# Kernel optimization log

Hardware: AMD Instinct MI355X
Metric: run time of the kernel (lower is better)

## Reference

```python
import jax, jax.numpy as jnp
import numpy as np

# BEV projection config (from model_cfg.PROJECT_CFG)
PCR = np.array([0.0, -40.0, -3.0, 70.4, 40.0, 1.0], dtype=np.float32)
VOX = np.array([0.16, 0.16, 4.0], dtype=np.float32)
NX = int(round((PCR[3] - PCR[0]) / VOX[0]))  # 440
NY = int(round((PCR[4] - PCR[1]) / VOX[1]))  # 500
NVOX = NX * NY


def setup_inputs() -> dict:
    key = jax.random.key(0)
    ks = jax.random.split(key, 7)
    B, C, H, W = 2, 32, 32, 256
    fv = jax.random.normal(ks[0], (B, C, H, W), jnp.float32)
    lo = jnp.array([0.0, -40.0, -3.0], jnp.float32).reshape(1, 3, 1, 1)
    hi = jnp.array([70.4, 40.0, 1.0], jnp.float32).reshape(1, 3, 1, 1)

    def mk_pts(k1, k2):
        xyz = lo + jax.random.uniform(k1, (B, 3, H, W), jnp.float32) * (hi - lo)
        inten = jax.random.uniform(k2, (B, 1, H, W), jnp.float32)
        return jnp.concatenate([xyz, inten], axis=1)

    points_img = mk_pts(ks[1], ks[2])
    points_img_far = mk_pts(ks[3], ks[4])
    proj_masks = jax.random.randint(ks[5], (B, H, W), 0, 2).astype(jnp.int32)
    proj_masks_far = jax.random.randint(ks[6], (B, H, W), 0, 2).astype(jnp.int32)
    return {
        "fv_features": fv,
        "points_img": points_img,
        "points_img_far": points_img_far,
        "proj_masks": proj_masks,
        "proj_masks_far": proj_masks_far,
    }


def _bev_scatter(points, feats, valid):
    """Scatter-mean per-point features into the BEV grid.

    points: (M, 3), feats: (M, C), valid: (M,) bool. Invalid / out-of-range
    points go to an overflow bucket that is dropped.
    """
    ix = jnp.floor((points[:, 0] - PCR[0]) / VOX[0]).astype(jnp.int32)
    iy = jnp.floor((points[:, 1] - PCR[1]) / VOX[1]).astype(jnp.int32)
    inb = (ix >= 0) & (ix < NX) & (iy >= 0) & (iy < NY)
    inb = inb & (points[:, 2] >= PCR[2]) & (points[:, 2] < PCR[5])
    ok = valid & inb
    seg = jnp.where(ok, iy * NX + ix, NVOX)
    fsum = jax.ops.segment_sum(jnp.where(ok[:, None], feats, 0.0), seg,
                               num_segments=NVOX + 1)
    cnt = jax.ops.segment_sum(ok.astype(feats.dtype), seg,
                              num_segments=NVOX + 1)
    mean = fsum[:NVOX] / jnp.maximum(cnt[:NVOX], 1.0)[:, None]
    return mean.reshape(NY, NX, -1).transpose(2, 0, 1)  # (C, NY, NX)


def reference(fv_features, points_img, points_img_far, proj_masks, proj_masks_far):
    B, C, H, W = fv_features.shape
    N = H * W
    feats = fv_features.transpose(0, 2, 3, 1).reshape(B, N, C)
    pts = points_img[:, :3].transpose(0, 2, 3, 1).reshape(B, N, 3)
    ptsf = points_img_far[:, :3].transpose(0, 2, 3, 1).reshape(B, N, 3)
    m = proj_masks.reshape(B, N) > 0      # valid near points (knowns)
    mf = proj_masks_far.reshape(B, N) > 0  # valid far points (unknowns)

    # three_nn: squared distances from far points to valid near points
    d2 = jnp.sum((ptsf[:, :, None, :] - pts[:, None, :, :]) ** 2, axis=-1)  # (B,N,N)
    d2 = jnp.where(m[:, None, :], d2, jnp.inf)
    neg, idx = jax.lax.top_k(-d2, 3)  # (B,N,3) three nearest
    dist = -neg
    dist_recip = 1.0 / (dist + 1e-8)
    weight = dist_recip / jnp.sum(dist_recip, axis=-1, keepdims=True)  # (B,N,3)

    # three_interpolate: weighted gather of near features
    gathered = jnp.take_along_axis(
        feats, idx.reshape(B, N * 3)[:, :, None], axis=1).reshape(B, N, 3, C)
    interp = jnp.sum(gathered * weight[..., None], axis=2)  # (B,N,C)

    # cat([features, interpolated]), cat([points, points_far]) -> BEV scatter
    all_pts = jnp.concatenate([pts, ptsf], axis=1)       # (B, 2N, 3)
    all_feats = jnp.concatenate([feats, interp], axis=1)  # (B, 2N, C)
    all_valid = jnp.concatenate([m, mf], axis=1)          # (B, 2N)
    bev = jax.vmap(_bev_scatter)(all_pts, all_feats, all_valid)  # (B,C,NY,NX)
    return bev
```

## Files before the change

### kernel.cpp

```cpp
#include <hip/hip_runtime.h>

#define BB   2
#define CC   32
#define NN   8192
#define N2   (2 * NN)
#define NXv  440
#define NYv  500
#define NVOXv (NXv * NYv)

#define SPLIT 32
#define FPB   8

#define INSERT3(dd, jj)                                            \
    if ((dd) < d2) {                                               \
        if ((dd) < d1) {                                           \
            d2 = d1; i2 = i1;                                      \
            if ((dd) < d0) { d1 = d0; i1 = i0; d0 = (dd); i0 = (jj); } \
            else           { d1 = (dd); i1 = (jj); }               \
        } else { d2 = (dd); i2 = (jj); }                           \
    }

__global__ __launch_bounds__(256) void k_tr(
    const float* __restrict__ fv, float* __restrict__ F,
    int* __restrict__ counters)
{
    __shared__ float tile[CC][64 + 1];
    int b  = blockIdx.y;
    int i0 = blockIdx.x * 64;
    int t  = threadIdx.x;
    if (b == 0 && blockIdx.x == 0 && t < 4) counters[t] = 0;

    const float* f = fv + (size_t)b * CC * NN;
    int il = t & 63, cb = t >> 6;
#pragma unroll
    for (int p = 0; p < 8; ++p) {
        int c = cb + p * 4;
        tile[c][il] = f[(size_t)c * NN + i0 + il];
    }
    __syncthreads();
    float* o = F + ((size_t)b * N2 + i0) * CC;
    int c2 = t & 31, ib = t >> 5;
#pragma unroll
    for (int p = 0; p < 8; ++p) {
        int il2 = ib + p * 8;
        o[(size_t)il2 * CC + c2] = tile[c2][il2];
    }
}

__global__ __launch_bounds__(256) void k_prep(
    const float* __restrict__ pim,
    const float* __restrict__ pimf,
    const int*   __restrict__ pm,
    const int*   __restrict__ pmf,
    int*         __restrict__ head,
    int*         __restrict__ nxt,
    float4*      __restrict__ cand,
    int*         __restrict__ ccnt,
    float4*      __restrict__ fcand,
    int*         __restrict__ fcnt)
{
    int b = blockIdx.y;
    int i = blockIdx.x * blockDim.x + threadIdx.x;

    {
        float x = pimf[(b * 4 + 0) * NN + i];
        float y = pimf[(b * 4 + 1) * NN + i];
        float z = pimf[(b * 4 + 2) * NN + i];
        if (pmf[b * NN + i] > 0) {
            int ix = (int)floorf((x - 0.0f)  / 0.16f);
            int iy = (int)floorf((y + 40.0f) / 0.16f);
            if (ix >= 0 && ix < NXv && iy >= 0 && iy < NYv &&
                z >= -3.0f && z < 1.0f) {
                int vox = iy * NXv + ix;
                int pos = atomicAdd(&fcnt[b], 1);
                fcand[b * NN + pos] = make_float4(x, y, z, __int_as_float(vox));
            }
        }
    }

    if (pm[b * NN + i] > 0) {
        float x = pim[(b * 4 + 0) * NN + i];
        float y = pim[(b * 4 + 1) * NN + i];
        float z = pim[(b * 4 + 2) * NN + i];
        int pos = atomicAdd(&ccnt[b], 1);
        cand[b * NN + pos] = make_float4(x, y, z, __int_as_float(i));

        int ix = (int)floorf((x - 0.0f)  / 0.16f);
        int iy = (int)floorf((y + 40.0f) / 0.16f);
        if (ix < 0 || ix >= NXv || iy < 0 || iy >= NYv) return;
        if (!(z >= -3.0f && z < 1.0f)) return;
        int vox = iy * NXv + ix;
        nxt[b * N2 + i] = atomicExch(&head[b * NVOXv + vox], i);
    }
}

__global__ __launch_bounds__(256) void k_far(
    const float4* __restrict__ cand,
    const int*    __restrict__ ccnt,
    const float4* __restrict__ fcand,
    const int*    __restrict__ fcnt,
    float*        __restrict__ F,
    int*          __restrict__ head,
    int*          __restrict__ nxt)
{
    int b  = blockIdx.y;
    int nf = fcnt[b];
    int e0 = blockIdx.x * FPB;
    if (e0 >= nf) return;

    int tid = threadIdx.x;
    int sub = tid & (SPLIT - 1);
    int e   = e0 + (tid >> 5);
    if (e >= nf) return;

    float4 fp = fcand[b * NN + e];
    float x = fp.x, y = fp.y, z = fp.z;
    int vox = __float_as_int(fp.w);

    int nc = ccnt[b];
    const float4* cb = cand + b * NN;

    float d0 = __builtin_inff(), d1 = __builtin_inff(), d2 = __builtin_inff();
    int   i0 = 0, i1 = 0, i2 = 0;

    int k = sub;
    for (; k + 96 < nc; k += 128) {
        float4 pa = cb[k];
        float4 pb = cb[k + 32];
        float4 pc = cb[k + 64];
        float4 pd = cb[k + 96];
        float dxa = x - pa.x, dya = y - pa.y, dza = z - pa.z;
        float dxb = x - pb.x, dyb = y - pb.y, dzb = z - pb.z;
        float dxc = x - pc.x, dyc = y - pc.y, dzc = z - pc.z;
        float dxd = x - pd.x, dyd = y - pd.y, dzd = z - pd.z;
        float da = dxa * dxa + dya * dya + dza * dza;
        float db = dxb * dxb + dyb * dyb + dzb * dzb;
        float dc = dxc * dxc + dyc * dyc + dzc * dzc;
        float dd = dxd * dxd + dyd * dyd + dzd * dzd;
        int ia = __float_as_int(pa.w);
        int ib = __float_as_int(pb.w);
        int ic = __float_as_int(pc.w);
        int id = __float_as_int(pd.w);
        INSERT3(da, ia);
        INSERT3(db, ib);
        INSERT3(dc, ic);
        INSERT3(dd, id);
    }
    for (; k < nc; k += SPLIT) {
        float4 p = cb[k];
        float dx = x - p.x, dy = y - p.y, dz = z - p.z;
        float d  = dx * dx + dy * dy + dz * dz;
        int  ii  = __float_as_int(p.w);
        INSERT3(d, ii);
    }

#pragma unroll
    for (int off = 1; off < SPLIT; off <<= 1) {
        float m0 = __shfl_xor(d0, off), m1 = __shfl_xor(d1, off), m2 = __shfl_xor(d2, off);
        int   g0 = __shfl_xor(i0, off), g1 = __shfl_xor(i1, off), g2 = __shfl_xor(i2, off);
        INSERT3(m0, g0);
        INSERT3(m1, g1);
        INSERT3(m2, g2);
    }

    float r0 = 1.0f / (d0 + 1e-8f);
    float r1 = 1.0f / (d1 + 1e-8f);
    float r2 = 1.0f / (d2 + 1e-8f);
    float s  = r0 + r1 + r2;
    float w0 = r0 / s, w1 = r1 / s, w2 = r2 / s;

    const float* fb = F + ((size_t)b * N2 << 5);
    float v = w0 * fb[((size_t)i0 << 5) + sub] +
              w1 * fb[((size_t)i1 << 5) + sub] +
              w2 * fb[((size_t)i2 << 5) + sub];
    F[(((size_t)b * N2 + NN + e) << 5) + sub] = v;

    if (sub == 0)
        nxt[b * N2 + NN + e] = atomicExch(&head[b * NVOXv + vox], NN + e);
}

__global__ __launch_bounds__(256) void k_final(
    const float* __restrict__ F,
    const int*   __restrict__ head,
    const int*   __restrict__ nxt,
    float*       __restrict__ out)
{
    __shared__ float tile[CC][64 + 1];
    int b  = blockIdx.y;
    int v0 = blockIdx.x * 64;
    int t  = threadIdx.x;

    int vl = t >> 2, cq = (t & 3) * 8;
    int v  = v0 + vl;
    float acc[8] = {0, 0, 0, 0, 0, 0, 0, 0};
    if (v < NVOXv) {
        int p = head[b * NVOXv + v];
        int n = 0;
        while (p >= 0) {
            const float* f = F + (((size_t)b * N2 + p) << 5) + cq;
            float4 a0 = *(const float4*)f;
            float4 a1 = *(const float4*)(f + 4);
            acc[0] += a0.x; acc[1] += a0.y; acc[2] += a0.z; acc[3] += a0.w;
            acc[4] += a1.x; acc[5] += a1.y; acc[6] += a1.z; acc[7] += a1.w;
            ++n;
            p = nxt[b * N2 + p];
        }
        if (n > 1) {
            float cf = (float)n;
#pragma unroll
            for (int u = 0; u < 8; ++u) acc[u] /= cf;
        }
    }
#pragma unroll
    for (int u = 0; u < 8; ++u) tile[cq + u][vl] = acc[u];
    __syncthreads();

    int c = t >> 3, vb = (t & 7) * 8;
    if (v0 + vb < NVOXv) {
        float* o = out + (size_t)b * CC * NVOXv + (size_t)c * NVOXv + v0 + vb;
        *(float4*)(o)     = make_float4(tile[c][vb + 0], tile[c][vb + 1],
                                        tile[c][vb + 2], tile[c][vb + 3]);
        *(float4*)(o + 4) = make_float4(tile[c][vb + 4], tile[c][vb + 5],
                                        tile[c][vb + 6], tile[c][vb + 7]);
    }
}

extern "C" void kernel_launch(void* const* d_in, const int* in_sizes, int n_in,
                              void* d_out, int out_size, void* d_ws, size_t ws_size,
                              hipStream_t stream)
{
    const float* fv   = (const float*)d_in[0];
    const float* pim  = (const float*)d_in[1];
    const float* pimf = (const float*)d_in[2];
    const int*   pm   = (const int*)d_in[3];
    const int*   pmf  = (const int*)d_in[4];
    float* out = (float*)d_out;

    const size_t headB = (size_t)BB * NVOXv * sizeof(int);
    const size_t nxtB  = (size_t)BB * N2 * sizeof(int);
    const size_t candB = (size_t)BB * NN * sizeof(float4);
    const size_t FB    = (size_t)BB * N2 * CC * sizeof(float);

    char* ws = (char*)d_ws;
    int* counters = (int*)ws;
    size_t off = 256;
    int*    head  = (int*)(ws + off);   off += headB;
    int*    nxt   = (int*)(ws + off);   off += nxtB;
    float4* cand  = (float4*)(ws + off); off += candB;
    float4* fcand = (float4*)(ws + off); off += candB;
    float*  F     = (float*)(ws + off);  off += FB;
    (void)ws_size;

    hipMemsetAsync(head, 0xFF, headB, stream);

    dim3 blk(256);
    dim3 gt(NN / 64, BB);
    k_tr<<<gt, blk, 0, stream>>>(fv, F, counters);

    dim3 g1(NN / 256, BB);
    k_prep<<<g1, blk, 0, stream>>>(pim, pimf, pm, pmf, head, nxt,
                                   cand, counters, fcand, counters + 2);

    dim3 g2(NN / FPB, BB);
    k_far<<<g2, blk, 0, stream>>>(cand, counters, fcand, counters + 2,
                                  F, head, nxt);

    dim3 g3((NVOXv + 63) / 64, BB);
    k_final<<<g3, blk, 0, stream>>>(F, head, nxt, out);
}
```

Baseline: 126.1 us.

## Fuse transpose and prep kernels, halve k_far split width, fold counter init into memset

Merges the feature transpose kernel and the point preparation kernel into one launch. Only the first 64 threads of each block do the prep work, so one kernel launch is removed. Counters are now reset by the same 0xFF memset that clears the head array, with a -1+1 offset trick on the atomic counters. k_far now uses 16 lanes per far point instead of 32 and handles 16 points per block, so each lane scans twice as many candidates and writes two channels. This trades cross-lane reduction steps for more serial distance work per lane.

```diff
diff --git a/kernel.cpp b/kernel.cpp
--- a/kernel.cpp
+++ b/kernel.cpp
@@ -8,8 +8,8 @@
 #define NYv  500
 #define NVOXv (NXv * NYv)
 
-#define SPLIT 32
-#define FPB   8
+#define SPLIT 16
+#define FPB   16
 
 #define INSERT3(dd, jj)                                            \
     if ((dd) < d2) {                                               \
@@ -20,15 +20,23 @@
         } else { d2 = (dd); i2 = (jj); }                           \
     }
 
-__global__ __launch_bounds__(256) void k_tr(
-    const float* __restrict__ fv, float* __restrict__ F,
-    int* __restrict__ counters)
+__global__ __launch_bounds__(256) void k_prep(
+    const float* __restrict__ fv,
+    const float* __restrict__ pim,
+    const float* __restrict__ pimf,
+    const int*   __restrict__ pm,
+    const int*   __restrict__ pmf,
+    float*       __restrict__ F,
+    int*         __restrict__ head,
+    int*         __restrict__ nxt,
+    float4*      __restrict__ cand,
+    int*         __restrict__ counters,
+    float4*      __restrict__ fcand)
 {
     __shared__ float tile[CC][64 + 1];
     int b  = blockIdx.y;
     int i0 = blockIdx.x * 64;
     int t  = threadIdx.x;
-    if (b == 0 && blockIdx.x == 0 && t < 4) counters[t] = 0;
 
     const float* f = fv + (size_t)b * CC * NN;
     int il = t & 63, cb = t >> 6;
@@ -45,90 +53,78 @@
         int il2 = ib + p * 8;
         o[(size_t)il2 * CC + c2] = tile[c2][il2];
     }
-}
-
-__global__ __launch_bounds__(256) void k_prep(
-    const float* __restrict__ pim,
-    const float* __restrict__ pimf,
-    const int*   __restrict__ pm,
-    const int*   __restrict__ pmf,
-    int*         __restrict__ head,
-    int*         __restrict__ nxt,
-    float4*      __restrict__ cand,
-    int*         __restrict__ ccnt,
-    float4*      __restrict__ fcand,
-    int*         __restrict__ fcnt)
-{
-    int b = blockIdx.y;
-    int i = blockIdx.x * blockDim.x + threadIdx.x;
-
-    {
-        float x = pimf[(b * 4 + 0) * NN + i];
-        float y = pimf[(b * 4 + 1) * NN + i];
-        float z = pimf[(b * 4 + 2) * NN + i];
-        if (pmf[b * NN + i] > 0) {
+
+    if (t < 64) {
+        int i = i0 + t;
+
+        {
+            float x = pimf[(b * 4 + 0) * NN + i];
+            float y = pimf[(b * 4 + 1) * NN + i];
+            float z = pimf[(b * 4 + 2) * NN + i];
+            if (pmf[b * NN + i] > 0) {
+                int ix = (int)floorf((x - 0.0f)  / 0.16f);
+                int iy = (int)floorf((y + 40.0f) / 0.16f);
+                if (ix >= 0 && ix < NXv && iy >= 0 && iy < NYv &&
+                    z >= -3.0f && z < 1.0f) {
+                    int vox = iy * NXv + ix;
+                    int pos = atomicAdd(&counters[2 + b], 1) + 1;
+                    fcand[b * NN + pos] = make_float4(x, y, z, __int_as_float(vox));
+                }
+            }
+        }
+
+        if (pm[b * NN + i] > 0) {
+            float x = pim[(b * 4 + 0) * NN + i];
+            float y = pim[(b * 4 + 1) * NN + i];
+            float z = pim[(b * 4 + 2) * NN + i];
+            int pos = atomicAdd(&counters[b], 1) + 1;
+            cand[b * NN + pos] = make_float4(x, y, z, __int_as_float(i));
+
             int ix = (int)floorf((x - 0.0f)  / 0.16f);
             int iy = (int)floorf((y + 40.0f) / 0.16f);
             if (ix >= 0 && ix < NXv && iy >= 0 && iy < NYv &&
                 z >= -3.0f && z < 1.0f) {
                 int vox = iy * NXv + ix;
-                int pos = atomicAdd(&fcnt[b], 1);
-                fcand[b * NN + pos] = make_float4(x, y, z, __int_as_float(vox));
+                nxt[b * N2 + i] = atomicExch(&head[b * NVOXv + vox], i);
             }
         }
-    }
-
-    if (pm[b * NN + i] > 0) {
-        float x = pim[(b * 4 + 0) * NN + i];
-        float y = pim[(b * 4 + 1) * NN + i];
-        float z = pim[(b * 4 + 2) * NN + i];
-        int pos = atomicAdd(&ccnt[b], 1);
-        cand[b * NN + pos] = make_float4(x, y, z, __int_as_float(i));
-
-        int ix = (int)floorf((x - 0.0f)  / 0.16f);
-        int iy = (int)floorf((y + 40.0f) / 0.16f);
-        if (ix < 0 || ix >= NXv || iy < 0 || iy >= NYv) return;
-        if (!(z >= -3.0f && z < 1.0f)) return;
-        int vox = iy * NXv + ix;
-        nxt[b * N2 + i] = atomicExch(&head[b * NVOXv + vox], i);
     }
 }
 
 __global__ __launch_bounds__(256) void k_far(
     const float4* __restrict__ cand,
-    const int*    __restrict__ ccnt,
+    const int*    __restrict__ counters,
     const float4* __restrict__ fcand,
-    const int*    __restrict__ fcnt,
     float*        __restrict__ F,
     int*          __restrict__ head,
     int*          __restrict__ nxt)
 {
     int b  = blockIdx.y;
-    int nf = fcnt[b];
+    int nf = counters[2 + b] + 1;
     int e0 = blockIdx.x * FPB;
     if (e0 >= nf) return;
 
     int tid = threadIdx.x;
     int sub = tid & (SPLIT - 1);
-    int e   = e0 + (tid >> 5);
+    int e   = e0 + (tid >> 4);
     if (e >= nf) return;
 
     float4 fp = fcand[b * NN + e];
     float x = fp.x, y = fp.y, z = fp.z;
     int vox = __float_as_int(fp.w);
 
-    int nc = ccnt[b];
+    int nc = counters[b] + 1;
     const float4* cb = cand + b * NN;
 
     float d0 = __builtin_inff(), d1 = __builtin_inff(), d2 = __builtin_inff();
     int   i0 = 0, i1 = 0, i2 = 0;
 
     int k = sub;
-    for (; k + 96 < nc; k += 128) {
+    for (; k + 48 < nc; k += 64) {
         float4 pa = cb[k];
-        float4 pb = cb[k + 32];
-        float4 pc = cb[k + 64];
-        float4 pd = cb[k + 96];
+        float4 pb = cb[k + 16];
+        float4 pc = cb[k + 32];
+        float4 pd = cb[k + 48];
         float dxa = x - pa.x, dya = y - pa.y, dza = z - pa.z;
         float dxb = x - pb.x, dyb = y - pb.y, dzb = z - pb.z;
         float dxc = x - pc.x, dyc = y - pc.y, dzc = z - pc.z;
@@ -170,10 +166,15 @@
     float w0 = r0 / s, w1 = r1 / s, w2 = r2 / s;
 
     const float* fb = F + ((size_t)b * N2 << 5);
-    float v = w0 * fb[((size_t)i0 << 5) + sub] +
-              w1 * fb[((size_t)i1 << 5) + sub] +
-              w2 * fb[((size_t)i2 << 5) + sub];
-    F[(((size_t)b * N2 + NN + e) << 5) + sub] = v;
+    float va = w0 * fb[((size_t)i0 << 5) + sub] +
+               w1 * fb[((size_t)i1 << 5) + sub] +
+               w2 * fb[((size_t)i2 << 5) + sub];
+    float vb = w0 * fb[((size_t)i0 << 5) + sub + 16] +
+               w1 * fb[((size_t)i1 << 5) + sub + 16] +
+               w2 * fb[((size_t)i2 << 5) + sub + 16];
+    size_t row = ((size_t)b * N2 + NN + e) << 5;
+    F[row + sub]      = va;
+    F[row + sub + 16] = vb;
 
     if (sub == 0)
         nxt[b * N2 + NN + e] = atomicExch(&head[b * NVOXv + vox], NN + e);
@@ -251,19 +252,15 @@
     float*  F     = (float*)(ws + off);  off += FB;
     (void)ws_size;
 
-    hipMemsetAsync(head, 0xFF, headB, stream);
+    hipMemsetAsync(d_ws, 0xFF, 256 + headB, stream);
 
     dim3 blk(256);
-    dim3 gt(NN / 64, BB);
-    k_tr<<<gt, blk, 0, stream>>>(fv, F, counters);
-
-    dim3 g1(NN / 256, BB);
-    k_prep<<<g1, blk, 0, stream>>>(pim, pimf, pm, pmf, head, nxt,
-                                   cand, counters, fcand, counters + 2);
+    dim3 g1(NN / 64, BB);
+    k_prep<<<g1, blk, 0, stream>>>(fv, pim, pimf, pm, pmf,
+                                   F, head, nxt, cand, counters, fcand);
 
     dim3 g2(NN / FPB, BB);
-    k_far<<<g2, blk, 0, stream>>>(cand, counters, fcand, counters + 2,
-                                  F, head, nxt);
+    k_far<<<g2, blk, 0, stream>>>(cand, counters, fcand, F, head, nxt);
 
     dim3 g3((NVOXv + 63) / 64, BB);
     k_final<<<g3, blk, 0, stream>>>(F, head, nxt, out);
```

After: 139.8 us. 10.8% more time.
